# Performance work log

Hardware: AMD Instinct MI355X
Metric: run time of the kernel (lower is better)

## Reference

```python
import jax, jax.numpy as jnp
import numpy as np

D_MODEL = 256
NUM_HEADS = 8
D_K = D_MODEL // NUM_HEADS
BATCH = 32
SEQ = 1024


def setup_inputs() -> dict:
    key = jax.random.key(0)
    ks = jax.random.split(key, 11)
    s = 1.0 / np.sqrt(D_MODEL)
    x = jax.random.normal(ks[0], (BATCH, SEQ, D_MODEL), dtype=jnp.float32)
    attn_mask = jax.random.randint(ks[1], (SEQ, SEQ), 0, 2) > 0  # bool topology mask
    # ensure self-attention allowed so no row is fully masked
    attn_mask = attn_mask | jnp.eye(SEQ, dtype=bool)
    Wq = jax.random.normal(ks[2], (D_MODEL, D_MODEL), jnp.float32) * s
    bq = jax.random.normal(ks[3], (D_MODEL,), jnp.float32) * s
    Wk = jax.random.normal(ks[4], (D_MODEL, D_MODEL), jnp.float32) * s
    bk = jax.random.normal(ks[5], (D_MODEL,), jnp.float32) * s
    Wv = jax.random.normal(ks[6], (D_MODEL, D_MODEL), jnp.float32) * s
    bv = jax.random.normal(ks[7], (D_MODEL,), jnp.float32) * s
    Wo = jax.random.normal(ks[8], (D_MODEL, D_MODEL), jnp.float32) * s
    bo = jax.random.normal(ks[9], (D_MODEL,), jnp.float32) * s
    return {"x": x, "attn_mask": attn_mask, "Wq": Wq, "bq": bq, "Wk": Wk,
            "bk": bk, "Wv": Wv, "bv": bv, "Wo": Wo, "bo": bo}


def reference(x, attn_mask, Wq, bq, Wk, bk, Wv, bv, Wo, bo):
    B, S, _ = x.shape
    scale = 1.0 / jnp.sqrt(jnp.asarray(D_K, x.dtype))
    def split_heads(t):  # (B,S,D) -> (B,H,S,d_k)
        return t.reshape(B, S, NUM_HEADS, D_K).transpose(0, 2, 1, 3)
    Q = split_heads(x @ Wq.T + bq)
    K = split_heads(x @ Wk.T + bk)
    V = split_heads(x @ Wv.T + bv)
    scores = jnp.einsum('bhqd,bhkd->bhqk', Q, K) * scale
    scores = jnp.where(attn_mask[None, None, :, :], scores, jnp.asarray(-1e9, scores.dtype))
    attn = jax.nn.softmax(scores, axis=-1)
    out = jnp.einsum('bhqk,bhkd->bhqd', attn, V)
    out = out.transpose(0, 2, 1, 3).reshape(B, S, D_MODEL)
    return out @ Wo.T + bo
```

## Files before the change

kernel.cpp:

```cpp
#include <hip/hip_runtime.h>
#include <hip/hip_fp16.h>
#include <stdint.h>

#define B_ 32
#define S_ 1024
#define DM 256
#define H_ 8

typedef _Float16 f16;
typedef _Float16 f16x8 __attribute__((ext_vector_type(8)));
typedef _Float16 f16x4 __attribute__((ext_vector_type(4)));
typedef float f32x4 __attribute__((ext_vector_type(4)));

static __device__ __forceinline__ void gload16(const void* g, void* lds) {
  __builtin_amdgcn_global_load_lds(
      (const __attribute__((address_space(1))) void*)(uintptr_t)g,
      (__attribute__((address_space(3))) void*)(uintptr_t)lds, 16, 0, 0);
}
static __device__ __forceinline__ float ex2(float x) {
  float r; asm("v_exp_f32 %0, %1" : "=v"(r) : "v"(x)); return r;
}
static __device__ __forceinline__ unsigned pkrtz(float a, float b) {
  unsigned r; asm("v_cvt_pkrtz_f16_f32 %0, %1, %2" : "=v"(r) : "v"(a), "v"(b)); return r;
}
static __device__ __forceinline__ unsigned pkmul(unsigned a, unsigned b) {
  unsigned r; asm("v_pk_mul_f16 %0, %1, %2" : "=v"(r) : "v"(a), "v"(b)); return r;
}

__global__ __launch_bounds__(256) void cvt_kernel(const float* __restrict__ in,
                                                  f16* __restrict__ out, int n4) {
  int i = blockIdx.x * blockDim.x + threadIdx.x;
  int stride = gridDim.x * blockDim.x;
  for (; i < n4; i += stride) {
    float4 v = reinterpret_cast<const float4*>(in)[i];
    f16x4 h = {(f16)v.x, (f16)v.y, (f16)v.z, (f16)v.w};
    reinterpret_cast<f16x4*>(out)[i] = h;
  }
}

__global__ __launch_bounds__(256) void expand_mask_kernel(const int* __restrict__ mask,
                                                          unsigned* __restrict__ pmx, int n) {
  int t = blockIdx.x * blockDim.x + threadIdx.x;
  if (t >= n) return;
  int2 mm = reinterpret_cast<const int2*>(mask)[t];
  pmx[t] = (mm.x ? 0x3C00u : 0u) | (mm.y ? 0x3C000000u : 0u);
}

__global__ __launch_bounds__(256) void qkv_gemm_kernel(
    const f16* __restrict__ xh, const f16* __restrict__ wh,
    const float* __restrict__ bq, const float* __restrict__ bk, const float* __restrict__ bv,
    f16* __restrict__ qh, f16* __restrict__ kh, f16* __restrict__ vth) {
  __shared__ __align__(16) f16 Al[128 * 32];
  __shared__ __align__(16) f16 Bl[128 * 32];
  const int tid = threadIdx.x;
  const int w = tid >> 6, l = tid & 63;
  const int mt = blockIdx.x / 6, nt = blockIdx.x % 6;
  const int mbase = mt * 128, nbase = nt * 128;
  const int wm = w >> 1, wn = w & 1;
  const int lg = l >> 4, lr = l & 15;
  f32x4 acc[4][4] = {};
  for (int ks = 0; ks < 8; ++ks) {
    __syncthreads();
#pragma unroll
    for (int j = 0; j < 2; ++j) {
      int c = (j * 4 + w) * 64 + l;
      gload16(xh + (size_t)(mbase + (c >> 2)) * 256 + ks * 32 + (c & 3) * 8,
              (char*)Al + (j * 4 + w) * 1024);
      gload16(wh + (size_t)(nbase + (c >> 2)) * 256 + ks * 32 + (c & 3) * 8,
              (char*)Bl + (j * 4 + w) * 1024);
    }
    __syncthreads();
    f16x8 af[4], bf[4];
#pragma unroll
    for (int i = 0; i < 4; ++i)
      af[i] = *(const f16x8*)((const char*)Al + (wm * 64 + i * 16 + lr) * 64 + lg * 16);
#pragma unroll
    for (int i = 0; i < 4; ++i)
      bf[i] = *(const f16x8*)((const char*)Bl + (wn * 64 + i * 16 + lr) * 64 + lg * 16);
#pragma unroll
    for (int mi = 0; mi < 4; ++mi)
#pragma unroll
      for (int ni = 0; ni < 4; ++ni)
        acc[mi][ni] = __builtin_amdgcn_mfma_f32_16x16x32_f16(af[mi], bf[ni], acc[mi][ni], 0, 0, 0);
  }
  const int proj = nt >> 1;
  const float* bias = proj == 0 ? bq : (proj == 1 ? bk : bv);
  const float qsc = 0.25504182524668425f;
#pragma unroll
  for (int mi = 0; mi < 4; ++mi) {
#pragma unroll
    for (int ni = 0; ni < 4; ++ni) {
      int n = nbase + wn * 64 + ni * 16 + lr;
      float bb = bias[n & 255];
#pragma unroll
      for (int r = 0; r < 4; ++r) {
        int m = mbase + wm * 64 + mi * 16 + lg * 4 + r;
        float val = acc[mi][ni][r] + bb;
        if (proj == 0) val *= qsc;
        f16 hv = (f16)val;
        int b = m >> 10, s = m & 1023;
        int hh = (n >> 5) & 7, d = n & 31;
        int bh = b * 8 + hh;
        if (proj == 0)      qh[((size_t)bh * 1024 + s) * 32 + d] = hv;
        else if (proj == 1) kh[((size_t)bh * 1024 + s) * 32 + d] = hv;
        else                vth[((size_t)bh * 32 + d) * 1024 + s] = hv;
      }
    }
  }
}

__global__ __launch_bounds__(256) void attn_kernel(
    const f16* __restrict__ qh, const f16* __restrict__ kh, const f16* __restrict__ vth,
    const unsigned* __restrict__ pmx, f16* __restrict__ attnh) {
  __shared__ __align__(16) f16 Kl[2][64 * 32];
  __shared__ __align__(16) f16 Vtl[2][32 * 64];
  __shared__ __align__(16) f16 Pl[4][16 * 64];
  const int tid = threadIdx.x;
  const int w = tid >> 6, l = tid & 63;
  const int bh = blockIdx.x >> 4, qt = blockIdx.x & 15;
  const int qbase = qt * 64;
  const int lg = l >> 4, lr = l & 15;
  const int q = qbase + w * 16 + lr;

  f16x8 qf = *(const f16x8*)(qh + ((size_t)bh * 1024 + q) * 32 + lg * 8);
  const unsigned* mrow = pmx + (size_t)q * 512;

  float mrun = -1e30f;
  f32x4 oacc[2] = {};
  f32x4 lacc = {};
  const f32x4 zero = {};
  f16x8 ones;
#pragma unroll
  for (int i = 0; i < 8; ++i) ones[i] = (f16)1.0f;

  const f16* kgbase = kh + ((size_t)bh * 1024 + (tid >> 2)) * 32 + (tid & 3) * 8;
  const f16* vgbase = vth + ((size_t)bh * 32 + (tid >> 3)) * 1024 + ((tid & 7) ^ ((tid >> 3) & 7)) * 8;

  uint2 mc[4], mn[4];
#pragma unroll
  for (int k = 0; k < 4; ++k) mc[k] = *(const uint2*)(mrow + 0 * 32 + k * 8 + lg * 2);
  gload16(kgbase, (char*)Kl[0] + tid * 16);
  gload16(vgbase, (char*)Vtl[0] + tid * 16);

  for (int t = 0; t < 16; ++t) {
    asm volatile("" ::: "memory");
    __builtin_amdgcn_s_barrier();
    const int nxt = t + 1;
    if (nxt < 16) {
#pragma unroll
      for (int k = 0; k < 4; ++k) mn[k] = *(const uint2*)(mrow + nxt * 32 + k * 8 + lg * 2);
      const int nb = nxt & 1;
      gload16(kgbase + (size_t)nxt * 64 * 32, (char*)Kl[nb] + tid * 16);
      gload16(vgbase + (size_t)nxt * 64, (char*)Vtl[nb] + tid * 16);
      asm volatile("s_waitcnt vmcnt(6)" ::: "memory");
    } else {
      asm volatile("s_waitcnt vmcnt(0)" ::: "memory");
    }
    __builtin_amdgcn_s_barrier();

    const char* kbuf = (const char*)Kl[t & 1];
    const char* vbuf = (const char*)Vtl[t & 1];

    f32x4 sc[4];
#pragma unroll
    for (int kt = 0; kt < 4; ++kt) {
      f16x8 kf = *(const f16x8*)(kbuf + (kt * 16 + lr) * 64 + lg * 16);
      sc[kt] = __builtin_amdgcn_mfma_f32_16x16x32_f16(kf, qf, zero, 0, 0, 0);
    }
    float t0 = fmaxf(fmaxf(sc[0][0], sc[0][1]), fmaxf(sc[0][2], sc[0][3]));
    float t1 = fmaxf(fmaxf(sc[1][0], sc[1][1]), fmaxf(sc[1][2], sc[1][3]));
    float t2 = fmaxf(fmaxf(sc[2][0], sc[2][1]), fmaxf(sc[2][2], sc[2][3]));
    float t3 = fmaxf(fmaxf(sc[3][0], sc[3][1]), fmaxf(sc[3][2], sc[3][3]));
    float pmax = fmaxf(fmaxf(t0, t1), fmaxf(t2, t3));
    pmax = fmaxf(pmax, __shfl_xor(pmax, 16));
    pmax = fmaxf(pmax, __shfl_xor(pmax, 32));
    if (__any(pmax > mrun + 8.0f)) {
      float mnew = fmaxf(mrun, pmax);
      float alpha = ex2(mrun - mnew);
      mrun = mnew;
#pragma unroll
      for (int r = 0; r < 4; ++r) {
        float ar = __shfl(alpha, (l & 48) | (lg * 4 + r), 64);
        oacc[0][r] *= ar;
        oacc[1][r] *= ar;
        lacc[r] *= ar;
      }
    }
    char* pbuf = (char*)Pl[w];
#pragma unroll
    for (int kt = 0; kt < 4; ++kt) {
      float p0 = ex2(sc[kt][0] - mrun);
      float p1 = ex2(sc[kt][1] - mrun);
      float p2 = ex2(sc[kt][2] - mrun);
      float p3 = ex2(sc[kt][3] - mrun);
      unsigned lo = pkmul(pkrtz(p0, p1), mc[kt].x);
      unsigned hi = pkmul(pkrtz(p2, p3), mc[kt].y);
      *(uint64_t*)(pbuf + lr * 128 + ((kt * 32 + lg * 8) ^ ((lr & 7) << 4))) =
          (uint64_t)lo | ((uint64_t)hi << 32);
    }
#pragma unroll
    for (int ss = 0; ss < 2; ++ss) {
      f16x8 pa = *(const f16x8*)(pbuf + lr * 128 + ((ss * 64 + lg * 16) ^ ((lr & 7) << 4)));
      lacc = __builtin_amdgcn_mfma_f32_16x16x32_f16(pa, ones, lacc, 0, 0, 0);
#pragma unroll
      for (int dt = 0; dt < 2; ++dt) {
        int vr = dt * 16 + lr;
        f16x8 vf = *(const f16x8*)(vbuf + vr * 128 + ((ss * 64 + lg * 16) ^ ((lr & 7) << 4)));
        oacc[dt] = __builtin_amdgcn_mfma_f32_16x16x32_f16(pa, vf, oacc[dt], 0, 0, 0);
      }
    }
#pragma unroll
    for (int k = 0; k < 4; ++k) mc[k] = mn[k];
  }

  const int b = bh >> 3, hh = bh & 7;
#pragma unroll
  for (int r = 0; r < 4; ++r) {
    float inv = 1.0f / lacc[r];
    int qrow = qbase + w * 16 + lg * 4 + r;
    size_t rowoff = ((size_t)b * 1024 + qrow) * 256 + hh * 32;
    attnh[rowoff + lr]      = (f16)(oacc[0][r] * inv);
    attnh[rowoff + 16 + lr] = (f16)(oacc[1][r] * inv);
  }
}

__global__ __launch_bounds__(256) void out_gemm_kernel(
    const f16* __restrict__ ah, const f16* __restrict__ wh,
    const float* __restrict__ bo, float* __restrict__ out) {
  __shared__ __align__(16) f16 Al[128 * 32];
  __shared__ __align__(16) f16 Bl[128 * 32];
  const int tid = threadIdx.x;
  const int w = tid >> 6, l = tid & 63;
  const int mt = blockIdx.x >> 1, nt = blockIdx.x & 1;
  const int mbase = mt * 128, nbase = nt * 128;
  const int wm = w >> 1, wn = w & 1;
  const int lg = l >> 4, lr = l & 15;
  f32x4 acc[4][4] = {};
  for (int ks = 0; ks < 8; ++ks) {
    __syncthreads();
#pragma unroll
    for (int j = 0; j < 2; ++j) {
      int c = (j * 4 + w) * 64 + l;
      gload16(ah + (size_t)(mbase + (c >> 2)) * 256 + ks * 32 + (c & 3) * 8,
              (char*)Al + (j * 4 + w) * 1024);
      gload16(wh + (size_t)(nbase + (c >> 2)) * 256 + ks * 32 + (c & 3) * 8,
              (char*)Bl + (j * 4 + w) * 1024);
    }
    __syncthreads();
    f16x8 af[4], bf[4];
#pragma unroll
    for (int i = 0; i < 4; ++i)
      af[i] = *(const f16x8*)((const char*)Al + (wm * 64 + i * 16 + lr) * 64 + lg * 16);
#pragma unroll
    for (int i = 0; i < 4; ++i)
      bf[i] = *(const f16x8*)((const char*)Bl + (wn * 64 + i * 16 + lr) * 64 + lg * 16);
#pragma unroll
    for (int mi = 0; mi < 4; ++mi)
#pragma unroll
      for (int ni = 0; ni < 4; ++ni)
        acc[mi][ni] = __builtin_amdgcn_mfma_f32_16x16x32_f16(af[mi], bf[ni], acc[mi][ni], 0, 0, 0);
  }
#pragma unroll
  for (int mi = 0; mi < 4; ++mi) {
#pragma unroll
    for (int ni = 0; ni < 4; ++ni) {
      int n = nbase + wn * 64 + ni * 16 + lr;
      float bb = bo[n];
#pragma unroll
      for (int r = 0; r < 4; ++r) {
        int m = mbase + wm * 64 + mi * 16 + lg * 4 + r;
        out[(size_t)m * 256 + n] = acc[mi][ni][r] + bb;
      }
    }
  }
}

extern "C" void kernel_launch(void* const* d_in, const int* in_sizes, int n_in,
                              void* d_out, int out_size, void* d_ws, size_t ws_size,
                              hipStream_t stream) {
  const float* x  = (const float*)d_in[0];
  const int* mask = (const int*)d_in[1];
  const float* Wq = (const float*)d_in[2];
  const float* bq = (const float*)d_in[3];
  const float* Wk = (const float*)d_in[4];
  const float* bk = (const float*)d_in[5];
  const float* Wv = (const float*)d_in[6];
  const float* bv = (const float*)d_in[7];
  const float* Wo = (const float*)d_in[8];
  const float* bo = (const float*)d_in[9];
  float* out = (float*)d_out;
  char* ws = (char*)d_ws;

  f16* xh    = (f16*)(ws);
  f16* attnh = (f16*)(ws);
  f16* qh    = (f16*)(ws + 16777216);
  f16* kh    = (f16*)(ws + 33554432);
  f16* vth   = (f16*)(ws + 50331648);
  f16* wqkvh = (f16*)(ws + 67108864);
  f16* woh   = (f16*)(ws + 67502080);
  unsigned* pmx = (unsigned*)(ws + 67633152);

  cvt_kernel<<<2048, 256, 0, stream>>>(x, xh, (B_*S_*DM) / 4);
  cvt_kernel<<<64, 256, 0, stream>>>(Wq, wqkvh, 16384);
  cvt_kernel<<<64, 256, 0, stream>>>(Wk, wqkvh + 65536, 16384);
  cvt_kernel<<<64, 256, 0, stream>>>(Wv, wqkvh + 131072, 16384);
  cvt_kernel<<<64, 256, 0, stream>>>(Wo, woh, 16384);
  expand_mask_kernel<<<2048, 256, 0, stream>>>(mask, pmx, 1024 * 512);
  qkv_gemm_kernel<<<1536, 256, 0, stream>>>(xh, wqkvh, bq, bk, bv, qh, kh, vth);
  attn_kernel<<<4096, 256, 0, stream>>>(qh, kh, vth, pmx, attnh);
  out_gemm_kernel<<<512, 256, 0, stream>>>(attnh, woh, bo, out);
}
```

Baseline: 309.3 us.

## Fuse prep kernels and widen attention KV tiles to 128 with XCD-aware block mapping

Six conversion and mask kernels are merged into one prep kernel to cut launch overhead. The attention kernel now processes 128-key tiles, fully unrolled over 8 iterations with double buffering. It also adds s_setprio around the MFMA sections, a launch-bounds occupancy hint, and a block-to-(batch,head) remapping that spreads heads across the dispatch order, likely to improve L2 locality per XCD. The larger LDS and register footprint may reduce occupancy. The weight conversion writes Wo contiguously after Wv, which assumes woh directly follows wqkvh in the workspace.

```diff
diff --git a/kernel.cpp b/kernel.cpp
--- a/kernel.cpp
+++ b/kernel.cpp
@@ -27,23 +27,28 @@
   unsigned r; asm("v_pk_mul_f16 %0, %1, %2" : "=v"(r) : "v"(a), "v"(b)); return r;
 }
 
-__global__ __launch_bounds__(256) void cvt_kernel(const float* __restrict__ in,
-                                                  f16* __restrict__ out, int n4) {
-  int i = blockIdx.x * blockDim.x + threadIdx.x;
-  int stride = gridDim.x * blockDim.x;
-  for (; i < n4; i += stride) {
-    float4 v = reinterpret_cast<const float4*>(in)[i];
+__global__ __launch_bounds__(256) void prep_kernel(
+    const float* __restrict__ x,
+    const float* __restrict__ Wq, const float* __restrict__ Wk,
+    const float* __restrict__ Wv, const float* __restrict__ Wo,
+    const int* __restrict__ mask,
+    f16* __restrict__ xh, f16* __restrict__ wh, unsigned* __restrict__ pmx) {
+  int idx = blockIdx.x * 256 + threadIdx.x;
+  if (idx < 2097152) {
+    float4 v = reinterpret_cast<const float4*>(x)[idx];
     f16x4 h = {(f16)v.x, (f16)v.y, (f16)v.z, (f16)v.w};
-    reinterpret_cast<f16x4*>(out)[i] = h;
-  }
-}
-
-__global__ __launch_bounds__(256) void expand_mask_kernel(const int* __restrict__ mask,
-                                                          unsigned* __restrict__ pmx, int n) {
-  int t = blockIdx.x * blockDim.x + threadIdx.x;
-  if (t >= n) return;
-  int2 mm = reinterpret_cast<const int2*>(mask)[t];
-  pmx[t] = (mm.x ? 0x3C00u : 0u) | (mm.y ? 0x3C000000u : 0u);
+    reinterpret_cast<f16x4*>(xh)[idx] = h;
+  } else if (idx < 2097152 + 65536) {
+    int j = idx - 2097152;
+    const float* src = j < 16384 ? Wq : j < 32768 ? Wk : j < 49152 ? Wv : Wo;
+    float4 v = reinterpret_cast<const float4*>(src)[j & 16383];
+    f16x4 h = {(f16)v.x, (f16)v.y, (f16)v.z, (f16)v.w};
+    reinterpret_cast<f16x4*>(wh)[j] = h;
+  } else {
+    int j = idx - (2097152 + 65536);
+    int2 mm = reinterpret_cast<const int2*>(mask)[j];
+    pmx[j] = (mm.x ? 0x3C00u : 0u) | (mm.y ? 0x3C000000u : 0u);
+  }
 }
 
 __global__ __launch_bounds__(256) void qkv_gemm_kernel(
@@ -99,25 +104,28 @@
         if (proj == 0) val *= qsc;
         f16 hv = (f16)val;
         int b = m >> 10, s = m & 1023;
-        int hh = (n >> 5) & 7, d = n & 31;
+        int hh = (n >> 5) & 7, dd = n & 31;
         int bh = b * 8 + hh;
-        if (proj == 0)      qh[((size_t)bh * 1024 + s) * 32 + d] = hv;
-        else if (proj == 1) kh[((size_t)bh * 1024 + s) * 32 + d] = hv;
-        else                vth[((size_t)bh * 32 + d) * 1024 + s] = hv;
+        if (proj == 0)      qh[((size_t)bh * 1024 + s) * 32 + dd] = hv;
+        else if (proj == 1) kh[((size_t)bh * 1024 + s) * 32 + dd] = hv;
+        else                vth[((size_t)bh * 32 + dd) * 1024 + s] = hv;
       }
     }
   }
 }
 
-__global__ __launch_bounds__(256) void attn_kernel(
+__global__ __launch_bounds__(256, 3) void attn_kernel(
     const f16* __restrict__ qh, const f16* __restrict__ kh, const f16* __restrict__ vth,
     const unsigned* __restrict__ pmx, f16* __restrict__ attnh) {
-  __shared__ __align__(16) f16 Kl[2][64 * 32];
-  __shared__ __align__(16) f16 Vtl[2][32 * 64];
-  __shared__ __align__(16) f16 Pl[4][16 * 64];
+  __shared__ __align__(16) f16 Kl[2][128 * 32];
+  __shared__ __align__(16) f16 Vtl[2][32 * 128];
+  __shared__ __align__(16) f16 Pl[4][16 * 128];
   const int tid = threadIdx.x;
   const int w = tid >> 6, l = tid & 63;
-  const int bh = blockIdx.x >> 4, qt = blockIdx.x & 15;
+  const int dsp = blockIdx.x;
+  const int slot = dsp >> 3;
+  const int bh = (slot >> 4) * 8 + (dsp & 7);
+  const int qt = slot & 15;
   const int qbase = qt * 64;
   const int lg = l >> 4, lr = l & 15;
   const int q = qbase + w * 16 + lr;
@@ -133,85 +141,98 @@
 #pragma unroll
   for (int i = 0; i < 8; ++i) ones[i] = (f16)1.0f;
 
-  const f16* kgbase = kh + ((size_t)bh * 1024 + (tid >> 2)) * 32 + (tid & 3) * 8;
-  const f16* vgbase = vth + ((size_t)bh * 32 + (tid >> 3)) * 1024 + ((tid & 7) ^ ((tid >> 3) & 7)) * 8;
-
-  uint2 mc[4], mn[4];
-#pragma unroll
-  for (int k = 0; k < 4; ++k) mc[k] = *(const uint2*)(mrow + 0 * 32 + k * 8 + lg * 2);
-  gload16(kgbase, (char*)Kl[0] + tid * 16);
-  gload16(vgbase, (char*)Vtl[0] + tid * 16);
-
-  for (int t = 0; t < 16; ++t) {
-    asm volatile("" ::: "memory");
-    __builtin_amdgcn_s_barrier();
-    const int nxt = t + 1;
-    if (nxt < 16) {
-#pragma unroll
-      for (int k = 0; k < 4; ++k) mn[k] = *(const uint2*)(mrow + nxt * 32 + k * 8 + lg * 2);
-      const int nb = nxt & 1;
-      gload16(kgbase + (size_t)nxt * 64 * 32, (char*)Kl[nb] + tid * 16);
-      gload16(vgbase + (size_t)nxt * 64, (char*)Vtl[nb] + tid * 16);
-      asm volatile("s_waitcnt vmcnt(6)" ::: "memory");
-    } else {
-      asm volatile("s_waitcnt vmcnt(0)" ::: "memory");
-    }
-    __builtin_amdgcn_s_barrier();
-
-    const char* kbuf = (const char*)Kl[t & 1];
-    const char* vbuf = (const char*)Vtl[t & 1];
-
-    f32x4 sc[4];
-#pragma unroll
-    for (int kt = 0; kt < 4; ++kt) {
-      f16x8 kf = *(const f16x8*)(kbuf + (kt * 16 + lr) * 64 + lg * 16);
-      sc[kt] = __builtin_amdgcn_mfma_f32_16x16x32_f16(kf, qf, zero, 0, 0, 0);
-    }
-    float t0 = fmaxf(fmaxf(sc[0][0], sc[0][1]), fmaxf(sc[0][2], sc[0][3]));
-    float t1 = fmaxf(fmaxf(sc[1][0], sc[1][1]), fmaxf(sc[1][2], sc[1][3]));
-    float t2 = fmaxf(fmaxf(sc[2][0], sc[2][1]), fmaxf(sc[2][2], sc[2][3]));
-    float t3 = fmaxf(fmaxf(sc[3][0], sc[3][1]), fmaxf(sc[3][2], sc[3][3]));
-    float pmax = fmaxf(fmaxf(t0, t1), fmaxf(t2, t3));
-    pmax = fmaxf(pmax, __shfl_xor(pmax, 16));
-    pmax = fmaxf(pmax, __shfl_xor(pmax, 32));
-    if (__any(pmax > mrun + 8.0f)) {
-      float mnew = fmaxf(mrun, pmax);
-      float alpha = ex2(mrun - mnew);
-      mrun = mnew;
-#pragma unroll
-      for (int r = 0; r < 4; ++r) {
-        float ar = __shfl(alpha, (l & 48) | (lg * 4 + r), 64);
-        oacc[0][r] *= ar;
-        oacc[1][r] *= ar;
-        lacc[r] *= ar;
-      }
-    }
-    char* pbuf = (char*)Pl[w];
-#pragma unroll
-    for (int kt = 0; kt < 4; ++kt) {
-      float p0 = ex2(sc[kt][0] - mrun);
-      float p1 = ex2(sc[kt][1] - mrun);
-      float p2 = ex2(sc[kt][2] - mrun);
-      float p3 = ex2(sc[kt][3] - mrun);
-      unsigned lo = pkmul(pkrtz(p0, p1), mc[kt].x);
-      unsigned hi = pkmul(pkrtz(p2, p3), mc[kt].y);
-      *(uint64_t*)(pbuf + lr * 128 + ((kt * 32 + lg * 8) ^ ((lr & 7) << 4))) =
-          (uint64_t)lo | ((uint64_t)hi << 32);
-    }
-#pragma unroll
-    for (int ss = 0; ss < 2; ++ss) {
-      f16x8 pa = *(const f16x8*)(pbuf + lr * 128 + ((ss * 64 + lg * 16) ^ ((lr & 7) << 4)));
-      lacc = __builtin_amdgcn_mfma_f32_16x16x32_f16(pa, ones, lacc, 0, 0, 0);
-#pragma unroll
-      for (int dt = 0; dt < 2; ++dt) {
-        int vr = dt * 16 + lr;
-        f16x8 vf = *(const f16x8*)(vbuf + vr * 128 + ((ss * 64 + lg * 16) ^ ((lr & 7) << 4)));
-        oacc[dt] = __builtin_amdgcn_mfma_f32_16x16x32_f16(pa, vf, oacc[dt], 0, 0, 0);
-      }
-    }
-#pragma unroll
-    for (int k = 0; k < 4; ++k) mc[k] = mn[k];
-  }
+  const f16* kg = kh + ((size_t)bh * 1024 + (tid >> 2)) * 32 + (tid & 3) * 8;
+  const int dv0 = tid >> 4, cb = tid & 15;
+  const f16* vg0 = vth + ((size_t)bh * 32 + dv0) * 1024 + (size_t)((cb ^ (dv0 & 7)) * 8);
+  char* kl0 = (char*)Kl[0];
+  char* kl1 = (char*)Kl[1];
+  char* vl0 = (char*)Vtl[0];
+  char* vl1 = (char*)Vtl[1];
+  char* pbuf = (char*)Pl[w];
+
+  uint2 mca[8], mcb[8];
+#pragma unroll
+  for (int k = 0; k < 8; ++k) mca[k] = *(const uint2*)(mrow + k * 8 + lg * 2);
+  gload16(kg, kl0 + tid * 16);
+  gload16(kg + 2048, kl0 + tid * 16 + 4096);
+  gload16(vg0, vl0 + tid * 16);
+  gload16(vg0 + 16 * 1024, vl0 + tid * 16 + 4096);
+
+#define DOTILE(T, KCUR, KNXT, VCUR, VNXT, MC, MN)                                   \
+  {                                                                                 \
+    asm volatile("s_waitcnt lgkmcnt(0)" ::: "memory");                              \
+    __builtin_amdgcn_s_barrier();                 \
+    if ((T) < 7) {                                                                  \
+      _Pragma("unroll") for (int k = 0; k < 8; ++k)                                 \
+          MN[k] = *(const uint2*)(mrow + ((T) + 1) * 64 + k * 8 + lg * 2);          \
+      gload16(kg + ((T) + 1) * 4096, (KNXT) + tid * 16);                            \
+      gload16(kg + ((T) + 1) * 4096 + 2048, (KNXT) + tid * 16 + 4096);              \
+      gload16(vg0 + ((T) + 1) * 128, (VNXT) + tid * 16);                            \
+      gload16(vg0 + 16 * 1024 + ((T) + 1) * 128, (VNXT) + tid * 16 + 4096);         \
+      asm volatile("s_waitcnt vmcnt(12)" ::: "memory");         \
+    } else {                                                                        \
+      asm volatile("s_waitcnt vmcnt(0)" ::: "memory");                              \
+    }                                                                               \
+    __builtin_amdgcn_s_barrier();               \
+    f32x4 sc[8];                                                                    \
+    __builtin_amdgcn_s_setprio(1);                                                  \
+    _Pragma("unroll") for (int kt = 0; kt < 8; ++kt) {                              \
+      f16x8 kf = *(const f16x8*)((KCUR) + (kt * 16 + lr) * 64 + lg * 16);           \
+      sc[kt] = __builtin_amdgcn_mfma_f32_16x16x32_f16(kf, qf, zero, 0, 0, 0);       \
+    }                                                                               \
+    __builtin_amdgcn_s_setprio(0);                                                  \
+    float m0 = fmaxf(fmaxf(sc[0][0], sc[0][1]), fmaxf(sc[0][2], sc[0][3]));         \
+    float m1 = fmaxf(fmaxf(sc[1][0], sc[1][1]), fmaxf(sc[1][2], sc[1][3]));         \
+    float m2 = fmaxf(fmaxf(sc[2][0], sc[2][1]), fmaxf(sc[2][2], sc[2][3]));         \
+    float m3 = fmaxf(fmaxf(sc[3][0], sc[3][1]), fmaxf(sc[3][2], sc[3][3]));         \
+    float m4 = fmaxf(fmaxf(sc[4][0], sc[4][1]), fmaxf(sc[4][2], sc[4][3]));         \
+    float m5 = fmaxf(fmaxf(sc[5][0], sc[5][1]), fmaxf(sc[5][2], sc[5][3]));         \
+    float m6 = fmaxf(fmaxf(sc[6][0], sc[6][1]), fmaxf(sc[6][2], sc[6][3]));         \
+    float m7 = fmaxf(fmaxf(sc[7][0], sc[7][1]), fmaxf(sc[7][2], sc[7][3]));         \
+    float pmax = fmaxf(fmaxf(fmaxf(m0, m1), fmaxf(m2, m3)),                         \
+                       fmaxf(fmaxf(m4, m5), fmaxf(m6, m7)));                        \
+    pmax = fmaxf(pmax, __shfl_xor(pmax, 16));                                       \
+    pmax = fmaxf(pmax, __shfl_xor(pmax, 32));                      \
+    if (__any(pmax > mrun + 8.0f)) {                                                \
+      float mnew = fmaxf(mrun, pmax);                                  \
+      float alpha = ex2(mrun - mnew);                                               \
+      mrun = mnew;                                                                  \
+      _Pragma("unroll") for (int r = 0; r < 4; ++r) {                               \
+        float ar = __shfl(alpha, (l & 48) | (lg * 4 + r), 64);                      \
+        oacc[0][r] *= ar; oacc[1][r] *= ar; lacc[r] *= ar;                          \
+      }                                                                             \
+    }                                                                               \
+    _Pragma("unroll") for (int kt = 0; kt < 8; ++kt) {                              \
+      float p0 = ex2(sc[kt][0] - mrun), p1 = ex2(sc[kt][1] - mrun);                 \
+      float p2 = ex2(sc[kt][2] - mrun), p3 = ex2(sc[kt][3] - mrun);                 \
+      unsigned lo = pkmul(pkrtz(p0, p1), MC[kt].x);                                 \
+      unsigned hi = pkmul(pkrtz(p2, p3), MC[kt].y);                                 \
+      *(uint64_t*)(pbuf + lr * 256 + ((kt * 32 + lg * 8) ^ ((lr & 7) << 4))) =      \
+          (uint64_t)lo | ((uint64_t)hi << 32);                                      \
+    }                                                                               \
+    __builtin_amdgcn_s_setprio(1);                                                  \
+    _Pragma("unroll") for (int ss = 0; ss < 4; ++ss) {                              \
+      f16x8 pa = *(const f16x8*)(pbuf + lr * 256 +                                  \
+                                 ((ss * 64 + lg * 16) ^ ((lr & 7) << 4)));          \
+      lacc = __builtin_amdgcn_mfma_f32_16x16x32_f16(pa, ones, lacc, 0, 0, 0);       \
+      _Pragma("unroll") for (int dt = 0; dt < 2; ++dt) {                            \
+        f16x8 vf = *(const f16x8*)((VCUR) + (dt * 16 + lr) * 256 +                  \
+                                   ((ss * 64 + lg * 16) ^ ((lr & 7) << 4)));        \
+        oacc[dt] = __builtin_amdgcn_mfma_f32_16x16x32_f16(pa, vf, oacc[dt], 0, 0, 0); \
+      }                                                                             \
+    }                                                                               \
+    __builtin_amdgcn_s_setprio(0);                                                  \
+  }
+
+  DOTILE(0, kl0, kl1, vl0, vl1, mca, mcb)
+  DOTILE(1, kl1, kl0, vl1, vl0, mcb, mca)
+  DOTILE(2, kl0, kl1, vl0, vl1, mca, mcb)
+  DOTILE(3, kl1, kl0, vl1, vl0, mcb, mca)
+  DOTILE(4, kl0, kl1, vl0, vl1, mca, mcb)
+  DOTILE(5, kl1, kl0, vl1, vl0, mcb, mca)
+  DOTILE(6, kl0, kl1, vl0, vl1, mca, mcb)
+  DOTILE(7, kl1, kl0, vl1, vl0, mcb, mca)
+#undef DOTILE
 
   const int b = bh >> 3, hh = bh & 7;
 #pragma unroll
@@ -300,12 +321,7 @@
   f16* woh   = (f16*)(ws + 67502080);
   unsigned* pmx = (unsigned*)(ws + 67633152);
 
-  cvt_kernel<<<2048, 256, 0, stream>>>(x, xh, (B_*S_*DM) / 4);
-  cvt_kernel<<<64, 256, 0, stream>>>(Wq, wqkvh, 16384);
-  cvt_kernel<<<64, 256, 0, stream>>>(Wk, wqkvh + 65536, 16384);
-  cvt_kernel<<<64, 256, 0, stream>>>(Wv, wqkvh + 131072, 16384);
-  cvt_kernel<<<64, 256, 0, stream>>>(Wo, woh, 16384);
-  expand_mask_kernel<<<2048, 256, 0, stream>>>(mask, pmx, 1024 * 512);
+  prep_kernel<<<10496, 256, 0, stream>>>(x, Wq, Wk, Wv, Wo, mask, xh, wqkvh, pmx);
   qkv_gemm_kernel<<<1536, 256, 0, stream>>>(xh, wqkvh, bq, bk, bv, qh, kh, vth);
   attn_kernel<<<4096, 256, 0, stream>>>(qh, kh, vth, pmx, attnh);
   out_gemm_kernel<<<512, 256, 0, stream>>>(attnh, woh, bo, out);
```

Measured after the change: 302.5 us. 2.2% less time.

## Merge prep kernels and load K/V straight to registers in attention

Applied to the files above, without the earlier changes.

Six conversion and mask-expansion launches are merged into one prep kernel with a single flat index space, cutting launch overhead. The attention kernel drops its LDS double-buffered K/V staging and both per-tile barriers, reading K and V fragments from global memory into registers and prefetching the next K tile. It also remaps block indices so that the eight heads of a batch run next to each other for L2 locality, sets a 4-wave occupancy hint, and raises wave priority around the MFMA sections. The trade-off is more global and L2 traffic per wave and higher register pressure, in exchange for no synchronisation stalls.

```diff
diff --git a/kernel.cpp b/kernel.cpp
--- a/kernel.cpp
+++ b/kernel.cpp
@@ -27,23 +27,28 @@
   unsigned r; asm("v_pk_mul_f16 %0, %1, %2" : "=v"(r) : "v"(a), "v"(b)); return r;
 }
 
-__global__ __launch_bounds__(256) void cvt_kernel(const float* __restrict__ in,
-                                                  f16* __restrict__ out, int n4) {
-  int i = blockIdx.x * blockDim.x + threadIdx.x;
-  int stride = gridDim.x * blockDim.x;
-  for (; i < n4; i += stride) {
-    float4 v = reinterpret_cast<const float4*>(in)[i];
+__global__ __launch_bounds__(256) void prep_kernel(
+    const float* __restrict__ x,
+    const float* __restrict__ Wq, const float* __restrict__ Wk,
+    const float* __restrict__ Wv, const float* __restrict__ Wo,
+    const int* __restrict__ mask,
+    f16* __restrict__ xh, f16* __restrict__ wh, unsigned* __restrict__ pmx) {
+  int idx = blockIdx.x * 256 + threadIdx.x;
+  if (idx < 2097152) {
+    float4 v = reinterpret_cast<const float4*>(x)[idx];
     f16x4 h = {(f16)v.x, (f16)v.y, (f16)v.z, (f16)v.w};
-    reinterpret_cast<f16x4*>(out)[i] = h;
-  }
-}
-
-__global__ __launch_bounds__(256) void expand_mask_kernel(const int* __restrict__ mask,
-                                                          unsigned* __restrict__ pmx, int n) {
-  int t = blockIdx.x * blockDim.x + threadIdx.x;
-  if (t >= n) return;
-  int2 mm = reinterpret_cast<const int2*>(mask)[t];
-  pmx[t] = (mm.x ? 0x3C00u : 0u) | (mm.y ? 0x3C000000u : 0u);
+    reinterpret_cast<f16x4*>(xh)[idx] = h;
+  } else if (idx < 2097152 + 65536) {
+    int j = idx - 2097152;
+    const float* src = j < 16384 ? Wq : j < 32768 ? Wk : j < 49152 ? Wv : Wo;
+    float4 v = reinterpret_cast<const float4*>(src)[j & 16383];
+    f16x4 h = {(f16)v.x, (f16)v.y, (f16)v.z, (f16)v.w};
+    reinterpret_cast<f16x4*>(wh)[j] = h;
+  } else {
+    int j = idx - (2097152 + 65536);
+    int2 mm = reinterpret_cast<const int2*>(mask)[j];
+    pmx[j] = (mm.x ? 0x3C00u : 0u) | (mm.y ? 0x3C000000u : 0u);
+  }
 }
 
 __global__ __launch_bounds__(256) void qkv_gemm_kernel(
@@ -99,31 +104,34 @@
         if (proj == 0) val *= qsc;
         f16 hv = (f16)val;
         int b = m >> 10, s = m & 1023;
-        int hh = (n >> 5) & 7, d = n & 31;
+        int hh = (n >> 5) & 7, dd = n & 31;
         int bh = b * 8 + hh;
-        if (proj == 0)      qh[((size_t)bh * 1024 + s) * 32 + d] = hv;
-        else if (proj == 1) kh[((size_t)bh * 1024 + s) * 32 + d] = hv;
-        else                vth[((size_t)bh * 32 + d) * 1024 + s] = hv;
+        if (proj == 0)      qh[((size_t)bh * 1024 + s) * 32 + dd] = hv;
+        else if (proj == 1) kh[((size_t)bh * 1024 + s) * 32 + dd] = hv;
+        else                vth[((size_t)bh * 32 + dd) * 1024 + s] = hv;
       }
     }
   }
 }
 
-__global__ __launch_bounds__(256) void attn_kernel(
+__global__ __launch_bounds__(256, 4) void attn_kernel(
     const f16* __restrict__ qh, const f16* __restrict__ kh, const f16* __restrict__ vth,
     const unsigned* __restrict__ pmx, f16* __restrict__ attnh) {
-  __shared__ __align__(16) f16 Kl[2][64 * 32];
-  __shared__ __align__(16) f16 Vtl[2][32 * 64];
   __shared__ __align__(16) f16 Pl[4][16 * 64];
   const int tid = threadIdx.x;
   const int w = tid >> 6, l = tid & 63;
-  const int bh = blockIdx.x >> 4, qt = blockIdx.x & 15;
+  const int dsp = blockIdx.x;
+  const int slot = dsp >> 3;
+  const int bh = (slot >> 4) * 8 + (dsp & 7);
+  const int qt = slot & 15;
   const int qbase = qt * 64;
   const int lg = l >> 4, lr = l & 15;
   const int q = qbase + w * 16 + lr;
 
   f16x8 qf = *(const f16x8*)(qh + ((size_t)bh * 1024 + q) * 32 + lg * 8);
   const unsigned* mrow = pmx + (size_t)q * 512;
+  const f16* kb = kh + (size_t)bh * 1024 * 32;
+  const f16* vb = vth + (size_t)bh * 32 * 1024;
 
   float mrun = -1e30f;
   f32x4 oacc[2] = {};
@@ -133,40 +141,40 @@
 #pragma unroll
   for (int i = 0; i < 8; ++i) ones[i] = (f16)1.0f;
 
-  const f16* kgbase = kh + ((size_t)bh * 1024 + (tid >> 2)) * 32 + (tid & 3) * 8;
-  const f16* vgbase = vth + ((size_t)bh * 32 + (tid >> 3)) * 1024 + ((tid & 7) ^ ((tid >> 3) & 7)) * 8;
-
-  uint2 mc[4], mn[4];
-#pragma unroll
-  for (int k = 0; k < 4; ++k) mc[k] = *(const uint2*)(mrow + 0 * 32 + k * 8 + lg * 2);
-  gload16(kgbase, (char*)Kl[0] + tid * 16);
-  gload16(vgbase, (char*)Vtl[0] + tid * 16);
-
+  char* pbuf = (char*)Pl[w];
+
+  f16x8 kf[2][4];
+#pragma unroll
+  for (int kt = 0; kt < 4; ++kt)
+    kf[0][kt] = *(const f16x8*)(kb + (size_t)(kt * 16 + lr) * 32 + lg * 8);
+
+#pragma unroll
   for (int t = 0; t < 16; ++t) {
-    asm volatile("" ::: "memory");
-    __builtin_amdgcn_s_barrier();
-    const int nxt = t + 1;
-    if (nxt < 16) {
-#pragma unroll
-      for (int k = 0; k < 4; ++k) mn[k] = *(const uint2*)(mrow + nxt * 32 + k * 8 + lg * 2);
-      const int nb = nxt & 1;
-      gload16(kgbase + (size_t)nxt * 64 * 32, (char*)Kl[nb] + tid * 16);
-      gload16(vgbase + (size_t)nxt * 64, (char*)Vtl[nb] + tid * 16);
-      asm volatile("s_waitcnt vmcnt(6)" ::: "memory");
-    } else {
-      asm volatile("s_waitcnt vmcnt(0)" ::: "memory");
-    }
-    __builtin_amdgcn_s_barrier();
-
-    const char* kbuf = (const char*)Kl[t & 1];
-    const char* vbuf = (const char*)Vtl[t & 1];
+    const int cur = t & 1, nxt = cur ^ 1;
+    const int kvb = t * 64;
+    if (t < 15) {
+#pragma unroll
+      for (int kt = 0; kt < 4; ++kt)
+        kf[nxt][kt] = *(const f16x8*)(kb + (size_t)(kvb + 64 + kt * 16 + lr) * 32 + lg * 8);
+    }
+    f16x8 vf[4];
+#pragma unroll
+    for (int ss = 0; ss < 2; ++ss)
+#pragma unroll
+      for (int dt = 0; dt < 2; ++dt)
+        vf[ss * 2 + dt] = *(const f16x8*)(vb + (size_t)(dt * 16 + lr) * 1024 + kvb + ss * 32 + lg * 8);
+    uint2 mc[4];
+#pragma unroll
+    for (int kt = 0; kt < 4; ++kt)
+      mc[kt] = *(const uint2*)(mrow + t * 32 + kt * 8 + lg * 2);
 
     f32x4 sc[4];
-#pragma unroll
-    for (int kt = 0; kt < 4; ++kt) {
-      f16x8 kf = *(const f16x8*)(kbuf + (kt * 16 + lr) * 64 + lg * 16);
-      sc[kt] = __builtin_amdgcn_mfma_f32_16x16x32_f16(kf, qf, zero, 0, 0, 0);
-    }
+    __builtin_amdgcn_s_setprio(1);
+#pragma unroll
+    for (int kt = 0; kt < 4; ++kt)
+      sc[kt] = __builtin_amdgcn_mfma_f32_16x16x32_f16(kf[cur][kt], qf, zero, 0, 0, 0);
+    __builtin_amdgcn_s_setprio(0);
+
     float t0 = fmaxf(fmaxf(sc[0][0], sc[0][1]), fmaxf(sc[0][2], sc[0][3]));
     float t1 = fmaxf(fmaxf(sc[1][0], sc[1][1]), fmaxf(sc[1][2], sc[1][3]));
     float t2 = fmaxf(fmaxf(sc[2][0], sc[2][1]), fmaxf(sc[2][2], sc[2][3]));
@@ -181,36 +189,28 @@
 #pragma unroll
       for (int r = 0; r < 4; ++r) {
         float ar = __shfl(alpha, (l & 48) | (lg * 4 + r), 64);
-        oacc[0][r] *= ar;
-        oacc[1][r] *= ar;
-        lacc[r] *= ar;
+        oacc[0][r] *= ar; oacc[1][r] *= ar; lacc[r] *= ar;
       }
     }
-    char* pbuf = (char*)Pl[w];
 #pragma unroll
     for (int kt = 0; kt < 4; ++kt) {
-      float p0 = ex2(sc[kt][0] - mrun);
-      float p1 = ex2(sc[kt][1] - mrun);
-      float p2 = ex2(sc[kt][2] - mrun);
-      float p3 = ex2(sc[kt][3] - mrun);
+      float p0 = ex2(sc[kt][0] - mrun), p1 = ex2(sc[kt][1] - mrun);
+      float p2 = ex2(sc[kt][2] - mrun), p3 = ex2(sc[kt][3] - mrun);
       unsigned lo = pkmul(pkrtz(p0, p1), mc[kt].x);
       unsigned hi = pkmul(pkrtz(p2, p3), mc[kt].y);
       *(uint64_t*)(pbuf + lr * 128 + ((kt * 32 + lg * 8) ^ ((lr & 7) << 4))) =
           (uint64_t)lo | ((uint64_t)hi << 32);
     }
+    __builtin_amdgcn_s_setprio(1);
 #pragma unroll
     for (int ss = 0; ss < 2; ++ss) {
       f16x8 pa = *(const f16x8*)(pbuf + lr * 128 + ((ss * 64 + lg * 16) ^ ((lr & 7) << 4)));
       lacc = __builtin_amdgcn_mfma_f32_16x16x32_f16(pa, ones, lacc, 0, 0, 0);
 #pragma unroll
-      for (int dt = 0; dt < 2; ++dt) {
-        int vr = dt * 16 + lr;
-        f16x8 vf = *(const f16x8*)(vbuf + vr * 128 + ((ss * 64 + lg * 16) ^ ((lr & 7) << 4)));
-        oacc[dt] = __builtin_amdgcn_mfma_f32_16x16x32_f16(pa, vf, oacc[dt], 0, 0, 0);
-      }
-    }
-#pragma unroll
-    for (int k = 0; k < 4; ++k) mc[k] = mn[k];
+      for (int dt = 0; dt < 2; ++dt)
+        oacc[dt] = __builtin_amdgcn_mfma_f32_16x16x32_f16(pa, vf[ss * 2 + dt], oacc[dt], 0, 0, 0);
+    }
+    __builtin_amdgcn_s_setprio(0);
   }
 
   const int b = bh >> 3, hh = bh & 7;
@@ -300,12 +300,7 @@
   f16* woh   = (f16*)(ws + 67502080);
   unsigned* pmx = (unsigned*)(ws + 67633152);
 
-  cvt_kernel<<<2048, 256, 0, stream>>>(x, xh, (B_*S_*DM) / 4);
-  cvt_kernel<<<64, 256, 0, stream>>>(Wq, wqkvh, 16384);
-  cvt_kernel<<<64, 256, 0, stream>>>(Wk, wqkvh + 65536, 16384);
-  cvt_kernel<<<64, 256, 0, stream>>>(Wv, wqkvh + 131072, 16384);
-  cvt_kernel<<<64, 256, 0, stream>>>(Wo, woh, 16384);
-  expand_mask_kernel<<<2048, 256, 0, stream>>>(mask, pmx, 1024 * 512);
+  prep_kernel<<<10496, 256, 0, stream>>>(x, Wq, Wk, Wv, Wo, mask, xh, wqkvh, pmx);
   qkv_gemm_kernel<<<1536, 256, 0, stream>>>(xh, wqkvh, bq, bk, bv, qh, kh, vth);
   attn_kernel<<<4096, 256, 0, stream>>>(qh, kh, vth, pmx, attnh);
   out_gemm_kernel<<<512, 256, 0, stream>>>(attnh, woh, bo, out);
```

Measured after the change: 444.6 us. +43.7%, slower.
